# Performance work log

Hardware: AMD Instinct MI355X
Metric: run time of the kernel (lower is better)

The kernel has to match this reference:

```python
import jax, jax.numpy as jnp
import numpy as np
from jax.ops import segment_sum

N_NODES = 100000
N_EDGES = 1600000
N_GRAPHS = 128
HIDDEN = 128
N_CLASSES = 10


def setup_inputs() -> dict:
    key = jax.random.key(0)
    ks = jax.random.split(key, 8)
    src = jax.random.randint(ks[0], (N_EDGES,), 0, N_NODES, dtype=jnp.int32)
    dst = jax.random.randint(ks[1], (N_EDGES,), 0, N_NODES, dtype=jnp.int32)
    graph_ids = jnp.sort(jax.random.randint(ks[2], (N_NODES,), 0, N_GRAPHS, dtype=jnp.int32))
    W1 = jax.random.normal(ks[3], (1, HIDDEN), dtype=jnp.float32)
    b1 = jnp.zeros((HIDDEN,), jnp.float32)
    W2 = jax.random.normal(ks[4], (HIDDEN, HIDDEN), dtype=jnp.float32) * 0.05
    b2 = jnp.zeros((HIDDEN,), jnp.float32)
    Wc = jax.random.normal(ks[5], (HIDDEN, N_CLASSES), dtype=jnp.float32) * 0.05
    bc = jnp.zeros((N_CLASSES,), jnp.float32)
    return {"src": src, "dst": dst, "graph_ids": graph_ids,
            "W1": W1, "b1": b1, "W2": W2, "b2": b2, "Wc": Wc, "bc": bc}


def _graph_conv(h, src, dst, norm_src, norm_dst, W, b, n_nodes):
    # DGL GraphConv, norm='both': D_out^{-1/2} gather -> scatter-sum -> W -> D_in^{-1/2} -> +b
    hs = h * norm_src[:, None]
    agg = segment_sum(hs[src], dst, num_segments=n_nodes)  # [N, F_in]
    return agg @ W * norm_dst[:, None] + b


def reference(src, dst, graph_ids, W1, b1, W2, b2, Wc, bc):
    n_nodes = graph_ids.shape[0]
    ones_e = jnp.ones(src.shape[0], jnp.float32)
    indeg = segment_sum(ones_e, dst, num_segments=n_nodes)
    outdeg = segment_sum(ones_e, src, num_segments=n_nodes)
    norm_src = jnp.clip(outdeg, 1.0, None) ** -0.5
    norm_dst = jnp.clip(indeg, 1.0, None) ** -0.5

    h = indeg[:, None]  # node feature = in-degree, [N, 1]
    h = jax.nn.relu(_graph_conv(h, src, dst, norm_src, norm_dst, W1, b1, n_nodes))
    h = jax.nn.relu(_graph_conv(h, src, dst, norm_src, norm_dst, W2, b2, n_nodes))

    # dgl.mean_nodes: per-graph mean pooling
    sums = segment_sum(h, graph_ids, num_segments=N_GRAPHS)          # [G, H]
    cnts = segment_sum(jnp.ones(n_nodes, jnp.float32), graph_ids, num_segments=N_GRAPHS)
    hg = sums / jnp.clip(cnts, 1.0, None)[:, None]
    return hg @ Wc + bc  # [G, n_classes]
```

## Files before the change

kernel.cpp:

```cpp
#include <hip/hip_runtime.h>

#define N_NODES   100000
#define N_EDGES   1600000
#define N_GRAPHS  128
#define HIDDEN    128
#define N_CLASSES 10

#define BSH   8
#define BSZ   256
#define NBUCK 391
#define NBIN  512
#define CAP   8192
#define PCH   4096
#define PTH   512
#define PIT   (PCH / PTH)

typedef unsigned int   uint;
typedef unsigned short ushort;

__device__ __forceinline__ uint scan_excl_512(uint v, int t, uint* wtmp) {
    uint lane = (uint)(t & 63);
    uint incl = v;
    #pragma unroll
    for (int off = 1; off < 64; off <<= 1) {
        uint up = __shfl_up(incl, off, 64);
        if (lane >= (uint)off) incl += up;
    }
    if (lane == 63) wtmp[t >> 6] = incl;
    __syncthreads();
    uint wo = 0;
    int w = t >> 6;
    #pragma unroll
    for (int k = 0; k < 7; ++k) wo += (k < w) ? wtmp[k] : 0u;
    __syncthreads();
    return incl + wo - v;
}

__global__ __launch_bounds__(PTH)
void k_part(const int* __restrict__ src, const int* __restrict__ dst,
            uint* __restrict__ bcur1, uint* __restrict__ bcur2,
            uint* __restrict__ tmp1, ushort* __restrict__ tmp2, int nE) {
    __shared__ uint   hist[NBIN], lcur[NBIN], base[NBIN];
    __shared__ uint   wtmp[8];
    __shared__ uint   stag4[PCH];
    __shared__ ushort stagB[PCH];
    int t = threadIdx.x;
    int e0 = blockIdx.x * PCH;
    int e1 = min(e0 + PCH, nE);
    int cntE = e1 - e0;

    int sv[PIT], dv[PIT];
    hist[t] = 0;
    __syncthreads();
    #pragma unroll
    for (int m = 0; m < PIT; ++m) {
        int e = e0 + t + m * PTH;
        if (e < e1) {
            sv[m] = src[e]; dv[m] = dst[e];
            atomicAdd(&hist[dv[m] >> BSH], 1u);
        }
    }
    __syncthreads();
    uint v = hist[t];
    uint excl = scan_excl_512(v, t, wtmp);
    lcur[t] = excl;
    if (v > 0) { uint g = atomicAdd(&bcur1[t], v); base[t] = (uint)t * CAP + g - excl; }
    __syncthreads();
    #pragma unroll
    for (int m = 0; m < PIT; ++m) {
        int e = e0 + t + m * PTH;
        if (e < e1) {
            int d = dv[m], s = sv[m];
            int b = d >> BSH;
            uint p = atomicAdd(&lcur[b], 1u);
            stag4[p] = ((uint)(d & (BSZ - 1)) << 17) | (uint)s;
            stagB[p] = (ushort)b;
        }
    }
    __syncthreads();
    for (int i = t; i < cntE; i += PTH) {
        uint b = stagB[i];
        uint a = base[b] + (uint)i;
        if (a < (b + 1u) * CAP) tmp1[a] = stag4[i];
    }
    __syncthreads();

    hist[t] = 0;
    __syncthreads();
    #pragma unroll
    for (int m = 0; m < PIT; ++m) {
        int e = e0 + t + m * PTH;
        if (e < e1) atomicAdd(&hist[sv[m] >> BSH], 1u);
    }
    __syncthreads();
    v = hist[t];
    excl = scan_excl_512(v, t, wtmp);
    lcur[t] = excl;
    if (v > 0) { uint g = atomicAdd(&bcur2[t], v); base[t] = (uint)t * CAP + g - excl; }
    __syncthreads();
    #pragma unroll
    for (int m = 0; m < PIT; ++m) {
        int e = e0 + t + m * PTH;
        if (e < e1) {
            int s = sv[m];
            uint p = atomicAdd(&lcur[s >> BSH], 1u);
            stag4[p] = (uint)s;
        }
    }
    __syncthreads();
    for (int i = t; i < cntE; i += PTH) {
        uint s = stag4[i];
        uint b = s >> BSH;
        uint a = base[b] + (uint)i;
        if (a < (b + 1u) * CAP) tmp2[a] = (ushort)(s & (BSZ - 1));
    }
}

__global__ __launch_bounds__(1024)
void k_cnt(const uint* __restrict__ bcur1, const uint* __restrict__ tmp1,
           const uint* __restrict__ bcur2, const ushort* __restrict__ tmp2,
           float* __restrict__ ns, float* __restrict__ hs0, float* __restrict__ ndv) {
    __shared__ uint cin[BSZ], cout[BSZ];
    int b = blockIdx.x, t = threadIdx.x;
    if (t < BSZ) { cin[t] = 0; cout[t] = 0; }
    __syncthreads();
    uint f1 = min(bcur1[b], (uint)CAP);
    const uint* tp1 = tmp1 + (size_t)b * CAP;
    uint i = t;
    for (; i + 3072u < f1; i += 4096u) {
        uint a0 = tp1[i], a1 = tp1[i + 1024], a2 = tp1[i + 2048], a3 = tp1[i + 3072];
        atomicAdd(&cin[a0 >> 17], 1u); atomicAdd(&cin[a1 >> 17], 1u);
        atomicAdd(&cin[a2 >> 17], 1u); atomicAdd(&cin[a3 >> 17], 1u);
    }
    for (; i < f1; i += 1024u) atomicAdd(&cin[tp1[i] >> 17], 1u);
    uint f2 = min(bcur2[b], (uint)CAP);
    const ushort* tp2 = tmp2 + (size_t)b * CAP;
    i = t;
    for (; i + 3072u < f2; i += 4096u) {
        uint a0 = tp2[i], a1 = tp2[i + 1024], a2 = tp2[i + 2048], a3 = tp2[i + 3072];
        atomicAdd(&cout[a0], 1u); atomicAdd(&cout[a1], 1u);
        atomicAdd(&cout[a2], 1u); atomicAdd(&cout[a3], 1u);
    }
    for (; i < f2; i += 1024u) atomicAdd(&cout[tp2[i]], 1u);
    __syncthreads();
    if (t < BSZ) {
        int n = b * BSZ + t;
        if (n < N_NODES) {
            uint ci = cin[t];
            float nsv = rsqrtf(fmaxf((float)cout[t], 1.0f));
            ns[n]  = nsv;
            hs0[n] = (float)ci * nsv;
            ndv[n] = rsqrtf(fmaxf((float)ci, 1.0f));
        }
    }
}

__global__ __launch_bounds__(1024)
void k_info(const uint* __restrict__ bcur1, const uint* __restrict__ tmp1,
            const float* __restrict__ hs0, const float* __restrict__ ns,
            const float* __restrict__ ndv,
            const float* __restrict__ W1, const float* __restrict__ b1,
            const float* __restrict__ W2,
            float* __restrict__ U, float* __restrict__ V,
            float4* __restrict__ info) {
    __shared__ float agg[BSZ];
    __shared__ float stu[128];
    __shared__ float sts[128];
    int b = blockIdx.x, t = threadIdx.x;
    if (t < BSZ) agg[t] = 0.0f;
    if (t < 128) {
        float w = W1[t], bb = b1[t];
        stu[t] = (w != 0.0f) ? (-bb / w) : 1e30f;
    }
    __syncthreads();
    if (b < 129) {
        if (t < 128) sts[t] = stu[t];
        __syncthreads();
        for (int k = 2; k <= 128; k <<= 1) {
            for (int j = k >> 1; j > 0; j >>= 1) {
                if (t < 128) {
                    int ixj = t ^ j;
                    if (ixj > t) {
                        float a = sts[t], bb = sts[ixj];
                        bool up = ((t & k) == 0);
                        if (up ? (a > bb) : (a < bb)) { sts[t] = bb; sts[ixj] = a; }
                    }
                }
                __syncthreads();
            }
        }
        if (t < 128) {
            int sg = b;
            float a_rep;
            if (sg == 0)        a_rep = sts[0]   - 1.0f;
            else if (sg == 128) a_rep = sts[127] + 1.0f;
            else                a_rep = 0.5f * (sts[sg - 1] + sts[sg]);
            float u = 0.0f, vv = 0.0f;
            #pragma unroll 8
            for (int j = 0; j < 128; ++j) {
                float w  = W1[j], bb = b1[j];
                float w2 = W2[j * HIDDEN + t];
                bool on  = (a_rep * w + bb > 0.0f);
                u  += on ? w  * w2 : 0.0f;
                vv += on ? bb * w2 : 0.0f;
            }
            U[sg * HIDDEN + t] = u;
            V[sg * HIDDEN + t] = vv;
        }
    }
    uint f1 = min(bcur1[b], (uint)CAP);
    const uint* tp1 = tmp1 + (size_t)b * CAP;
    uint i = t;
    for (; i + 3072u < f1; i += 4096u) {
        uint e0 = tp1[i], e1 = tp1[i + 1024], e2 = tp1[i + 2048], e3 = tp1[i + 3072];
        float h0 = hs0[e0 & 0x1FFFFu], h1 = hs0[e1 & 0x1FFFFu];
        float h2 = hs0[e2 & 0x1FFFFu], h3 = hs0[e3 & 0x1FFFFu];
        atomicAdd(&agg[e0 >> 17], h0); atomicAdd(&agg[e1 >> 17], h1);
        atomicAdd(&agg[e2 >> 17], h2); atomicAdd(&agg[e3 >> 17], h3);
    }
    for (; i < f1; i += 1024u) {
        uint e = tp1[i];
        atomicAdd(&agg[e >> 17], hs0[e & 0x1FFFFu]);
    }
    __syncthreads();
    int n = b * BSZ + t;
    if (t < BSZ && n < N_NODES) {
        float nd = ndv[n];
        float av = agg[t] * nd;
        int sgp = 0;
        #pragma unroll 16
        for (int q = 0; q < 128; ++q) sgp += (stu[q] < av) ? 1 : 0;
        float nsv = ns[n];
        info[n] = make_float4(nsv * av, nsv, __int_as_float(sgp), nd);
    }
}

__global__ __launch_bounds__(1024)
void k_conv2(const uint* __restrict__ bcur1, const uint* __restrict__ tmp1,
             const float4* __restrict__ info, const float* __restrict__ ndv,
             const float* __restrict__ U, const float* __restrict__ V,
             const int* __restrict__ graph_ids, const float* __restrict__ b2,
             float* __restrict__ pool, float* __restrict__ cnt) {
    __shared__ float aggA[BSZ], aggB[BSZ];
    __shared__ uint  smn[BSZ], smx[BSZ];
    int b = blockIdx.x, t = threadIdx.x;
    if (t < BSZ) { aggA[t] = 0.0f; aggB[t] = 0.0f; smn[t] = 255u; smx[t] = 0u; }
    __syncthreads();
    uint f1 = min(bcur1[b], (uint)CAP);
    const uint* tp1 = tmp1 + (size_t)b * CAP;
    uint i = t;
    for (; i + 3072u < f1; i += 4096u) {
        uint e0 = tp1[i], e1 = tp1[i + 1024], e2 = tp1[i + 2048], e3 = tp1[i + 3072];
        float4 n0 = info[e0 & 0x1FFFFu];
        float4 n1 = info[e1 & 0x1FFFFu];
        float4 n2 = info[e2 & 0x1FFFFu];
        float4 n3 = info[e3 & 0x1FFFFu];
        uint d0 = e0 >> 17, d1 = e1 >> 17, d2 = e2 >> 17, d3 = e3 >> 17;
        atomicAdd(&aggA[d0], n0.x); atomicAdd(&aggB[d0], n0.y);
        atomicAdd(&aggA[d1], n1.x); atomicAdd(&aggB[d1], n1.y);
        atomicAdd(&aggA[d2], n2.x); atomicAdd(&aggB[d2], n2.y);
        atomicAdd(&aggA[d3], n3.x); atomicAdd(&aggB[d3], n3.y);
        uint s0 = (uint)__float_as_int(n0.z), s1 = (uint)__float_as_int(n1.z);
        uint s2 = (uint)__float_as_int(n2.z), s3 = (uint)__float_as_int(n3.z);
        atomicMin(&smn[d0], s0); atomicMax(&smx[d0], s0);
        atomicMin(&smn[d1], s1); atomicMax(&smx[d1], s1);
        atomicMin(&smn[d2], s2); atomicMax(&smx[d2], s2);
        atomicMin(&smn[d3], s3); atomicMax(&smx[d3], s3);
    }
    for (; i < f1; i += 1024u) {
        uint e = tp1[i];
        uint dl = e >> 17;
        float4 nf = info[e & 0x1FFFFu];
        atomicAdd(&aggA[dl], nf.x);
        atomicAdd(&aggB[dl], nf.y);
        uint sg = (uint)__float_as_int(nf.z);
        atomicMin(&smn[dl], sg);
        atomicMax(&smx[dl], sg);
    }
    __syncthreads();

    int d = t & 127, q = t >> 7;
    float bbd = b2[d];
    int base = b * BSZ;
    int nmax = min(BSZ, N_NODES - base);
    int gcur = -1; float racc = 0.0f, cl = 0.0f;
    for (int r = q; r < nmax; r += 8) {
        int n = base + r;
        uint mn = smn[r], mx = smx[r];
        float acc;
        if (mn >= mx) {
            uint sg = min(mn, 128u);
            acc = aggA[r] * U[sg * HIDDEN + d] + aggB[r] * V[sg * HIDDEN + d];
        } else {
            acc = 0.0f;
            for (uint k = 0; k < f1; ++k) {
                uint e = tp1[k];
                if ((e >> 17) == (uint)r) {
                    float4 nf = info[e & 0x1FFFFu];
                    uint sg = (uint)__float_as_int(nf.z);
                    acc += nf.x * U[sg * HIDDEN + d] + nf.y * V[sg * HIDDEN + d];
                }
            }
        }
        float nd = ndv[n];
        float row = fmaxf(nd * acc + bbd, 0.0f);
        int g = graph_ids[n];
        if (g != gcur) {
            if (gcur >= 0) {
                atomicAdd(&pool[gcur * HIDDEN + d], racc);
                if (d == 0) atomicAdd(&cnt[gcur], cl);
            }
            gcur = g; racc = 0.0f; cl = 0.0f;
        }
        racc += row; cl += 1.0f;
    }
    if (gcur >= 0) {
        atomicAdd(&pool[gcur * HIDDEN + d], racc);
        if (d == 0) atomicAdd(&cnt[gcur], cl);
    }
}

__global__ void k_final(const float* __restrict__ pool, const float* __restrict__ cnt,
                        const float* __restrict__ Wc, const float* __restrict__ bc,
                        float* __restrict__ out) {
    int t = blockIdx.x * blockDim.x + threadIdx.x;
    if (t >= N_GRAPHS * N_CLASSES) return;
    int g = t / N_CLASSES, c = t % N_CLASSES;
    float inv = 1.0f / fmaxf(cnt[g], 1.0f);
    float acc = bc[c];
    for (int j = 0; j < HIDDEN; ++j)
        acc += pool[g * HIDDEN + j] * inv * Wc[j * N_CLASSES + c];
    out[t] = acc;
}

extern "C" void kernel_launch(void* const* d_in, const int* in_sizes, int n_in,
                              void* d_out, int out_size, void* d_ws, size_t ws_size,
                              hipStream_t stream) {
    const int*   src       = (const int*)d_in[0];
    const int*   dst       = (const int*)d_in[1];
    const int*   graph_ids = (const int*)d_in[2];
    const float* W1        = (const float*)d_in[3];
    const float* b1        = (const float*)d_in[4];
    const float* W2        = (const float*)d_in[5];
    const float* b2        = (const float*)d_in[6];
    const float* Wc        = (const float*)d_in[7];
    const float* bc        = (const float*)d_in[8];
    float* out = (float*)d_out;

    char* ws = (char*)d_ws;
    size_t off = 0;
    auto alloc = [&](size_t elems) { void* p = ws + off; off += elems * 4; return p; };

    uint*  bcur1 = (uint*) alloc(NBIN);
    uint*  bcur2 = (uint*) alloc(NBIN);
    float* pool  = (float*)alloc(N_GRAPHS * HIDDEN);
    float* cnt   = (float*)alloc(N_GRAPHS);
    size_t zero_bytes = off;
    float4* info = (float4*)alloc((size_t)N_NODES * 4);
    uint*   tmp1 = (uint*)  alloc((size_t)NBUCK * CAP);
    ushort* tmp2 = (ushort*)alloc((size_t)NBUCK * CAP / 2);
    float*  nsA  = (float*) alloc(N_NODES);
    float*  hs0  = (float*) alloc(N_NODES);
    float*  ndv  = (float*) alloc(N_NODES);
    float*  U    = (float*) alloc(129 * HIDDEN);
    float*  V    = (float*) alloc(129 * HIDDEN);

    hipMemsetAsync(d_ws, 0, zero_bytes, stream);

    int pblocks = (N_EDGES + PCH - 1) / PCH;
    k_part <<<pblocks, PTH, 0, stream>>>(src, dst, bcur1, bcur2, tmp1, tmp2, N_EDGES);
    k_cnt  <<<NBUCK, 1024, 0, stream>>>(bcur1, tmp1, bcur2, tmp2, nsA, hs0, ndv);
    k_info <<<NBUCK, 1024, 0, stream>>>(bcur1, tmp1, hs0, nsA, ndv, W1, b1, W2, U, V, info);
    k_conv2<<<NBUCK, 1024, 0, stream>>>(bcur1, tmp1, info, ndv, U, V, graph_ids, b2, pool, cnt);
    k_final<<<(N_GRAPHS * N_CLASSES + 255) / 256, 256, 0, stream>>>(pool, cnt, Wc, bc, out);
}
```

Baseline: 175.0 us.

## Split per-bucket edge aggregation across four blocks and add separate node passes

Each 256-node bucket's edge list is now processed by four 256-thread blocks instead of one 1024-thread block. Partial results are merged into global per-node arrays with atomics, and separate node-wise kernels compute norms and per-node info. Pooling is moved to its own kernel over 128-node chunks, with shared-memory staging of per-graph partial sums. The goal is more blocks in flight across the CUs on a launch that had only 391 blocks. The cost is extra kernel launches, global atomics, and round trips of intermediate arrays through memory.

```diff
diff --git a/kernel.cpp b/kernel.cpp
--- a/kernel.cpp
+++ b/kernel.cpp
@@ -9,11 +9,13 @@
 #define BSH   8
 #define BSZ   256
 #define NBUCK 391
+#define NPAD  (NBUCK * BSZ)
 #define NBIN  512
 #define CAP   8192
 #define PCH   4096
 #define PTH   512
 #define PIT   (PCH / PTH)
+#define SPLIT 4
 
 typedef unsigned int   uint;
 typedef unsigned short ushort;
@@ -116,65 +118,55 @@
     }
 }
 
-__global__ __launch_bounds__(1024)
-void k_cnt(const uint* __restrict__ bcur1, const uint* __restrict__ tmp1,
-           const uint* __restrict__ bcur2, const ushort* __restrict__ tmp2,
-           float* __restrict__ ns, float* __restrict__ hs0, float* __restrict__ ndv) {
-    __shared__ uint cin[BSZ], cout[BSZ];
-    int b = blockIdx.x, t = threadIdx.x;
-    if (t < BSZ) { cin[t] = 0; cout[t] = 0; }
+__global__ __launch_bounds__(256)
+void k_cnt4(const uint* __restrict__ bcur1, const uint* __restrict__ tmp1,
+            const uint* __restrict__ bcur2, const ushort* __restrict__ tmp2,
+            uint* __restrict__ cin, uint* __restrict__ cout) {
+    __shared__ uint lin[BSZ], lout[BSZ];
+    int b = blockIdx.x >> 2, q = blockIdx.x & 3;
+    int t = threadIdx.x;
+    lin[t] = 0; lout[t] = 0;
     __syncthreads();
     uint f1 = min(bcur1[b], (uint)CAP);
+    uint lo = f1 * (uint)q / 4u, hi = f1 * (uint)(q + 1) / 4u;
     const uint* tp1 = tmp1 + (size_t)b * CAP;
-    uint i = t;
-    for (; i + 3072u < f1; i += 4096u) {
-        uint a0 = tp1[i], a1 = tp1[i + 1024], a2 = tp1[i + 2048], a3 = tp1[i + 3072];
-        atomicAdd(&cin[a0 >> 17], 1u); atomicAdd(&cin[a1 >> 17], 1u);
-        atomicAdd(&cin[a2 >> 17], 1u); atomicAdd(&cin[a3 >> 17], 1u);
-    }
-    for (; i < f1; i += 1024u) atomicAdd(&cin[tp1[i] >> 17], 1u);
+    uint i = lo + t;
+    for (; i + 768u < hi; i += 1024u) {
+        uint a0 = tp1[i], a1 = tp1[i + 256], a2 = tp1[i + 512], a3 = tp1[i + 768];
+        atomicAdd(&lin[a0 >> 17], 1u); atomicAdd(&lin[a1 >> 17], 1u);
+        atomicAdd(&lin[a2 >> 17], 1u); atomicAdd(&lin[a3 >> 17], 1u);
+    }
+    for (; i < hi; i += 256u) atomicAdd(&lin[tp1[i] >> 17], 1u);
+
     uint f2 = min(bcur2[b], (uint)CAP);
+    uint lo2 = f2 * (uint)q / 4u, hi2 = f2 * (uint)(q + 1) / 4u;
     const ushort* tp2 = tmp2 + (size_t)b * CAP;
-    i = t;
-    for (; i + 3072u < f2; i += 4096u) {
-        uint a0 = tp2[i], a1 = tp2[i + 1024], a2 = tp2[i + 2048], a3 = tp2[i + 3072];
-        atomicAdd(&cout[a0], 1u); atomicAdd(&cout[a1], 1u);
-        atomicAdd(&cout[a2], 1u); atomicAdd(&cout[a3], 1u);
-    }
-    for (; i < f2; i += 1024u) atomicAdd(&cout[tp2[i]], 1u);
-    __syncthreads();
-    if (t < BSZ) {
-        int n = b * BSZ + t;
-        if (n < N_NODES) {
-            uint ci = cin[t];
-            float nsv = rsqrtf(fmaxf((float)cout[t], 1.0f));
-            ns[n]  = nsv;
-            hs0[n] = (float)ci * nsv;
-            ndv[n] = rsqrtf(fmaxf((float)ci, 1.0f));
-        }
-    }
-}
-
-__global__ __launch_bounds__(1024)
-void k_info(const uint* __restrict__ bcur1, const uint* __restrict__ tmp1,
-            const float* __restrict__ hs0, const float* __restrict__ ns,
-            const float* __restrict__ ndv,
-            const float* __restrict__ W1, const float* __restrict__ b1,
-            const float* __restrict__ W2,
-            float* __restrict__ U, float* __restrict__ V,
-            float4* __restrict__ info) {
-    __shared__ float agg[BSZ];
-    __shared__ float stu[128];
+    i = lo2 + t;
+    for (; i + 768u < hi2; i += 1024u) {
+        uint a0 = tp2[i], a1 = tp2[i + 256], a2 = tp2[i + 512], a3 = tp2[i + 768];
+        atomicAdd(&lout[a0], 1u); atomicAdd(&lout[a1], 1u);
+        atomicAdd(&lout[a2], 1u); atomicAdd(&lout[a3], 1u);
+    }
+    for (; i < hi2; i += 256u) atomicAdd(&lout[tp2[i]], 1u);
+    __syncthreads();
+    int n = b * BSZ + t;
+    if (lin[t])  atomicAdd(&cin[n],  lin[t]);
+    if (lout[t]) atomicAdd(&cout[n], lout[t]);
+}
+
+__global__ __launch_bounds__(256)
+void k_node1(const uint* __restrict__ cin, const uint* __restrict__ cout,
+             const float* __restrict__ W1, const float* __restrict__ b1,
+             const float* __restrict__ W2,
+             float* __restrict__ ns, float* __restrict__ hs0, float* __restrict__ ndv,
+             float* __restrict__ aggC, float* __restrict__ U, float* __restrict__ V) {
     __shared__ float sts[128];
     int b = blockIdx.x, t = threadIdx.x;
-    if (t < BSZ) agg[t] = 0.0f;
-    if (t < 128) {
-        float w = W1[t], bb = b1[t];
-        stu[t] = (w != 0.0f) ? (-bb / w) : 1e30f;
-    }
-    __syncthreads();
     if (b < 129) {
-        if (t < 128) sts[t] = stu[t];
+        if (t < 128) {
+            float w = W1[t], bb = b1[t];
+            sts[t] = (w != 0.0f) ? (-bb / w) : 1e30f;
+        }
         __syncthreads();
         for (int k = 2; k <= 128; k <<= 1) {
             for (int j = k >> 1; j > 0; j >>= 1) {
@@ -208,115 +200,199 @@
             V[sg * HIDDEN + t] = vv;
         }
     }
+    int n = b * 256 + t;
+    uint ci = cin[n];
+    float nsv = rsqrtf(fmaxf((float)cout[n], 1.0f));
+    ns[n]   = nsv;
+    hs0[n]  = (float)ci * nsv;
+    ndv[n]  = rsqrtf(fmaxf((float)ci, 1.0f));
+    aggC[n] = 0.0f;
+}
+
+__global__ __launch_bounds__(256)
+void k_agg1(const uint* __restrict__ bcur1, const uint* __restrict__ tmp1,
+            const float* __restrict__ hs0, float* __restrict__ aggC) {
+    __shared__ float agg[BSZ];
+    int b = blockIdx.x >> 2, q = blockIdx.x & 3;
+    int t = threadIdx.x;
+    agg[t] = 0.0f;
+    __syncthreads();
     uint f1 = min(bcur1[b], (uint)CAP);
+    uint lo = f1 * (uint)q / 4u, hi = f1 * (uint)(q + 1) / 4u;
     const uint* tp1 = tmp1 + (size_t)b * CAP;
-    uint i = t;
-    for (; i + 3072u < f1; i += 4096u) {
-        uint e0 = tp1[i], e1 = tp1[i + 1024], e2 = tp1[i + 2048], e3 = tp1[i + 3072];
+    uint i = lo + t;
+    for (; i + 768u < hi; i += 1024u) {
+        uint e0 = tp1[i], e1 = tp1[i + 256], e2 = tp1[i + 512], e3 = tp1[i + 768];
         float h0 = hs0[e0 & 0x1FFFFu], h1 = hs0[e1 & 0x1FFFFu];
         float h2 = hs0[e2 & 0x1FFFFu], h3 = hs0[e3 & 0x1FFFFu];
         atomicAdd(&agg[e0 >> 17], h0); atomicAdd(&agg[e1 >> 17], h1);
         atomicAdd(&agg[e2 >> 17], h2); atomicAdd(&agg[e3 >> 17], h3);
     }
-    for (; i < f1; i += 1024u) {
+    for (; i < hi; i += 256u) {
         uint e = tp1[i];
         atomicAdd(&agg[e >> 17], hs0[e & 0x1FFFFu]);
     }
     __syncthreads();
-    int n = b * BSZ + t;
-    if (t < BSZ && n < N_NODES) {
-        float nd = ndv[n];
-        float av = agg[t] * nd;
-        int sgp = 0;
-        #pragma unroll 16
-        for (int q = 0; q < 128; ++q) sgp += (stu[q] < av) ? 1 : 0;
-        float nsv = ns[n];
-        info[n] = make_float4(nsv * av, nsv, __int_as_float(sgp), nd);
-    }
-}
-
-__global__ __launch_bounds__(1024)
-void k_conv2(const uint* __restrict__ bcur1, const uint* __restrict__ tmp1,
-             const float4* __restrict__ info, const float* __restrict__ ndv,
-             const float* __restrict__ U, const float* __restrict__ V,
-             const int* __restrict__ graph_ids, const float* __restrict__ b2,
-             float* __restrict__ pool, float* __restrict__ cnt) {
-    __shared__ float aggA[BSZ], aggB[BSZ];
-    __shared__ uint  smn[BSZ], smx[BSZ];
-    int b = blockIdx.x, t = threadIdx.x;
-    if (t < BSZ) { aggA[t] = 0.0f; aggB[t] = 0.0f; smn[t] = 255u; smx[t] = 0u; }
+    if (agg[t] != 0.0f) atomicAdd(&aggC[b * BSZ + t], agg[t]);
+}
+
+__global__ __launch_bounds__(256)
+void k_node2(const float* __restrict__ aggC, const float* __restrict__ ns,
+             const float* __restrict__ ndv,
+             const float* __restrict__ W1, const float* __restrict__ b1,
+             float4* __restrict__ info, float* __restrict__ aggA,
+             float* __restrict__ aggB, uint* __restrict__ aggMn,
+             uint* __restrict__ aggMx) {
+    __shared__ float stu[128];
+    int t = threadIdx.x;
+    if (t < 128) {
+        float w = W1[t], bb = b1[t];
+        stu[t] = (w != 0.0f) ? (-bb / w) : 1e30f;
+    }
+    __syncthreads();
+    int n = blockIdx.x * 256 + t;
+    float nd = ndv[n];
+    float av = aggC[n] * nd;
+    int sgp = 0;
+    #pragma unroll 16
+    for (int q = 0; q < 128; ++q) sgp += (stu[q] < av) ? 1 : 0;
+    float nsv = ns[n];
+    info[n] = make_float4(nsv * av, nsv, __int_as_float(sgp), nd);
+    aggA[n] = 0.0f; aggB[n] = 0.0f; aggMn[n] = 255u; aggMx[n] = 0u;
+}
+
+__global__ __launch_bounds__(256)
+void k_agg2(const uint* __restrict__ bcur1, const uint* __restrict__ tmp1,
+            const float4* __restrict__ info,
+            float* __restrict__ aggA, float* __restrict__ aggB,
+            uint* __restrict__ aggMn, uint* __restrict__ aggMx) {
+    __shared__ float lA[BSZ], lB[BSZ];
+    __shared__ uint  lmn[BSZ], lmx[BSZ];
+    int b = blockIdx.x >> 2, q = blockIdx.x & 3;
+    int t = threadIdx.x;
+    lA[t] = 0.0f; lB[t] = 0.0f; lmn[t] = 255u; lmx[t] = 0u;
     __syncthreads();
     uint f1 = min(bcur1[b], (uint)CAP);
+    uint lo = f1 * (uint)q / 4u, hi = f1 * (uint)(q + 1) / 4u;
     const uint* tp1 = tmp1 + (size_t)b * CAP;
-    uint i = t;
-    for (; i + 3072u < f1; i += 4096u) {
-        uint e0 = tp1[i], e1 = tp1[i + 1024], e2 = tp1[i + 2048], e3 = tp1[i + 3072];
+    uint i = lo + t;
+    for (; i + 768u < hi; i += 1024u) {
+        uint e0 = tp1[i], e1 = tp1[i + 256], e2 = tp1[i + 512], e3 = tp1[i + 768];
         float4 n0 = info[e0 & 0x1FFFFu];
         float4 n1 = info[e1 & 0x1FFFFu];
         float4 n2 = info[e2 & 0x1FFFFu];
         float4 n3 = info[e3 & 0x1FFFFu];
         uint d0 = e0 >> 17, d1 = e1 >> 17, d2 = e2 >> 17, d3 = e3 >> 17;
-        atomicAdd(&aggA[d0], n0.x); atomicAdd(&aggB[d0], n0.y);
-        atomicAdd(&aggA[d1], n1.x); atomicAdd(&aggB[d1], n1.y);
-        atomicAdd(&aggA[d2], n2.x); atomicAdd(&aggB[d2], n2.y);
-        atomicAdd(&aggA[d3], n3.x); atomicAdd(&aggB[d3], n3.y);
+        atomicAdd(&lA[d0], n0.x); atomicAdd(&lB[d0], n0.y);
+        atomicAdd(&lA[d1], n1.x); atomicAdd(&lB[d1], n1.y);
+        atomicAdd(&lA[d2], n2.x); atomicAdd(&lB[d2], n2.y);
+        atomicAdd(&lA[d3], n3.x); atomicAdd(&lB[d3], n3.y);
         uint s0 = (uint)__float_as_int(n0.z), s1 = (uint)__float_as_int(n1.z);
         uint s2 = (uint)__float_as_int(n2.z), s3 = (uint)__float_as_int(n3.z);
-        atomicMin(&smn[d0], s0); atomicMax(&smx[d0], s0);
-        atomicMin(&smn[d1], s1); atomicMax(&smx[d1], s1);
-        atomicMin(&smn[d2], s2); atomicMax(&smx[d2], s2);
-        atomicMin(&smn[d3], s3); atomicMax(&smx[d3], s3);
-    }
-    for (; i < f1; i += 1024u) {
+        atomicMin(&lmn[d0], s0); atomicMax(&lmx[d0], s0);
+        atomicMin(&lmn[d1], s1); atomicMax(&lmx[d1], s1);
+        atomicMin(&lmn[d2], s2); atomicMax(&lmx[d2], s2);
+        atomicMin(&lmn[d3], s3); atomicMax(&lmx[d3], s3);
+    }
+    for (; i < hi; i += 256u) {
         uint e = tp1[i];
         uint dl = e >> 17;
         float4 nf = info[e & 0x1FFFFu];
-        atomicAdd(&aggA[dl], nf.x);
-        atomicAdd(&aggB[dl], nf.y);
+        atomicAdd(&lA[dl], nf.x);
+        atomicAdd(&lB[dl], nf.y);
         uint sg = (uint)__float_as_int(nf.z);
-        atomicMin(&smn[dl], sg);
-        atomicMax(&smx[dl], sg);
-    }
-    __syncthreads();
-
-    int d = t & 127, q = t >> 7;
-    float bbd = b2[d];
-    int base = b * BSZ;
-    int nmax = min(BSZ, N_NODES - base);
+        atomicMin(&lmn[dl], sg);
+        atomicMax(&lmx[dl], sg);
+    }
+    __syncthreads();
+    if (lmn[t] <= lmx[t]) {
+        int n = b * BSZ + t;
+        atomicAdd(&aggA[n], lA[t]);
+        atomicAdd(&aggB[n], lB[t]);
+        atomicMin(&aggMn[n], lmn[t]);
+        atomicMax(&aggMx[n], lmx[t]);
+    }
+}
+
+__global__ __launch_bounds__(256)
+void k_pool(const uint* __restrict__ bcur1, const uint* __restrict__ tmp1,
+            const float4* __restrict__ info, const float* __restrict__ ndv,
+            const float* __restrict__ aggA, const float* __restrict__ aggB,
+            const uint* __restrict__ aggMn, const uint* __restrict__ aggMx,
+            const float* __restrict__ U, const float* __restrict__ V,
+            const int* __restrict__ graph_ids, const float* __restrict__ b2,
+            float* __restrict__ pool, float* __restrict__ cnt) {
+    __shared__ float psl[4][HIDDEN];
+    __shared__ float csl[4];
+    __shared__ uint  tfl[4];
+    __shared__ int   g0s;
+    int t = threadIdx.x;
+    int d = t & 127, j = t >> 7;
+    int nb = blockIdx.x * 128;
+    if (t < 4) { csl[t] = 0.0f; tfl[t] = 0u; }
+    for (int s = t; s < 4 * HIDDEN; s += 256) ((float*)psl)[s] = 0.0f;
+    if (t == 0) g0s = graph_ids[nb];
+    __syncthreads();
+    int g0 = g0s;
+    float b2d = b2[d];
     int gcur = -1; float racc = 0.0f, cl = 0.0f;
-    for (int r = q; r < nmax; r += 8) {
-        int n = base + r;
-        uint mn = smn[r], mx = smx[r];
+    for (int r = j; r < 128; r += 2) {
+        int n = nb + r;
+        if (n >= N_NODES) break;
+        uint mn = aggMn[n], mx = aggMx[n];
         float acc;
         if (mn >= mx) {
             uint sg = min(mn, 128u);
-            acc = aggA[r] * U[sg * HIDDEN + d] + aggB[r] * V[sg * HIDDEN + d];
+            acc = aggA[n] * U[sg * HIDDEN + d] + aggB[n] * V[sg * HIDDEN + d];
         } else {
             acc = 0.0f;
+            int bb = n >> BSH;
+            uint f1 = min(bcur1[bb], (uint)CAP);
+            const uint* tp1 = tmp1 + (size_t)bb * CAP;
+            uint dl = (uint)(n & (BSZ - 1));
             for (uint k = 0; k < f1; ++k) {
                 uint e = tp1[k];
-                if ((e >> 17) == (uint)r) {
+                if ((e >> 17) == dl) {
                     float4 nf = info[e & 0x1FFFFu];
                     uint sg = (uint)__float_as_int(nf.z);
                     acc += nf.x * U[sg * HIDDEN + d] + nf.y * V[sg * HIDDEN + d];
                 }
             }
         }
-        float nd = ndv[n];
-        float row = fmaxf(nd * acc + bbd, 0.0f);
+        float row = fmaxf(ndv[n] * acc + b2d, 0.0f);
         int g = graph_ids[n];
         if (g != gcur) {
             if (gcur >= 0) {
-                atomicAdd(&pool[gcur * HIDDEN + d], racc);
-                if (d == 0) atomicAdd(&cnt[gcur], cl);
+                int slot = gcur - g0;
+                if (slot >= 0 && slot < 4) {
+                    atomicAdd(&psl[slot][d], racc);
+                    if (d == 0) { atomicAdd(&csl[slot], cl); tfl[slot] = 1u; }
+                } else {
+                    atomicAdd(&pool[gcur * HIDDEN + d], racc);
+                    if (d == 0) atomicAdd(&cnt[gcur], cl);
+                }
             }
             gcur = g; racc = 0.0f; cl = 0.0f;
         }
         racc += row; cl += 1.0f;
     }
     if (gcur >= 0) {
-        atomicAdd(&pool[gcur * HIDDEN + d], racc);
-        if (d == 0) atomicAdd(&cnt[gcur], cl);
+        int slot = gcur - g0;
+        if (slot >= 0 && slot < 4) {
+            atomicAdd(&psl[slot][d], racc);
+            if (d == 0) { atomicAdd(&csl[slot], cl); tfl[slot] = 1u; }
+        } else {
+            atomicAdd(&pool[gcur * HIDDEN + d], racc);
+            if (d == 0) atomicAdd(&cnt[gcur], cl);
+        }
+    }
+    __syncthreads();
+    #pragma unroll
+    for (int s = 0; s < 4; ++s) {
+        if (tfl[s]) {
+            if (t < 128) atomicAdd(&pool[(g0 + s) * HIDDEN + t], psl[s][t]);
+            if (t == 128) atomicAdd(&cnt[g0 + s], csl[s]);
+        }
     }
 }
 
@@ -355,22 +431,37 @@
     uint*  bcur2 = (uint*) alloc(NBIN);
     float* pool  = (float*)alloc(N_GRAPHS * HIDDEN);
     float* cnt   = (float*)alloc(N_GRAPHS);
+    uint*  cin   = (uint*) alloc(NPAD);
+    uint*  cout  = (uint*) alloc(NPAD);
     size_t zero_bytes = off;
-    float4* info = (float4*)alloc((size_t)N_NODES * 4);
-    uint*   tmp1 = (uint*)  alloc((size_t)NBUCK * CAP);
-    ushort* tmp2 = (ushort*)alloc((size_t)NBUCK * CAP / 2);
-    float*  nsA  = (float*) alloc(N_NODES);
-    float*  hs0  = (float*) alloc(N_NODES);
-    float*  ndv  = (float*) alloc(N_NODES);
-    float*  U    = (float*) alloc(129 * HIDDEN);
-    float*  V    = (float*) alloc(129 * HIDDEN);
+    float4* info  = (float4*)alloc((size_t)NPAD * 4);
+    uint*   tmp1  = (uint*)  alloc((size_t)NBUCK * CAP);
+    ushort* tmp2  = (ushort*)alloc((size_t)NBUCK * CAP / 2);
+    float*  nsA   = (float*) alloc(NPAD);
+    float*  hs0   = (float*) alloc(NPAD);
+    float*  ndv   = (float*) alloc(NPAD);
+    float*  aggC  = (float*) alloc(NPAD);
+    float*  aggA  = (float*) alloc(NPAD);
+    float*  aggB  = (float*) alloc(NPAD);
+    uint*   aggMn = (uint*)  alloc(NPAD);
+    uint*   aggMx = (uint*)  alloc(NPAD);
+    float*  U     = (float*) alloc(129 * HIDDEN);
+    float*  V     = (float*) alloc(129 * HIDDEN);
 
     hipMemsetAsync(d_ws, 0, zero_bytes, stream);
 
     int pblocks = (N_EDGES + PCH - 1) / PCH;
+    int gblocks = NBUCK * SPLIT;
+    int nblocks = NPAD / 256;
+    int oblocks = NPAD / 128;
+
     k_part <<<pblocks, PTH, 0, stream>>>(src, dst, bcur1, bcur2, tmp1, tmp2, N_EDGES);
-    k_cnt  <<<NBUCK, 1024, 0, stream>>>(bcur1, tmp1, bcur2, tmp2, nsA, hs0, ndv);
-    k_info <<<NBUCK, 1024, 0, stream>>>(bcur1, tmp1, hs0, nsA, ndv, W1, b1, W2, U, V, info);
-    k_conv2<<<NBUCK, 1024, 0, stream>>>(bcur1, tmp1, info, ndv, U, V, graph_ids, b2, pool, cnt);
+    k_cnt4 <<<gblocks, 256, 0, stream>>>(bcur1, tmp1, bcur2, tmp2, cin, cout);
+    k_node1<<<nblocks, 256, 0, stream>>>(cin, cout, W1, b1, W2, nsA, hs0, ndv, aggC, U, V);
+    k_agg1 <<<gblocks, 256, 0, stream>>>(bcur1, tmp1, hs0, aggC);
+    k_node2<<<nblocks, 256, 0, stream>>>(aggC, nsA, ndv, W1, b1, info, aggA, aggB, aggMn, aggMx);
+    k_agg2 <<<gblocks, 256, 0, stream>>>(bcur1, tmp1, info, aggA, aggB, aggMn, aggMx);
+    k_pool <<<oblocks, 256, 0, stream>>>(bcur1, tmp1, info, ndv, aggA, aggB, aggMn, aggMx,
+                                         U, V, graph_ids, b2, pool, cnt);
     k_final<<<(N_GRAPHS * N_CLASSES + 255) / 256, 256, 0, stream>>>(pool, cnt, Wc, bc, out);
 }
```

Measured after the change: 188.8 us. 1.08x slower.

## Shrink node buckets to 64 nodes and pack out-degree indices into bytes

Applied to the files above, without the earlier changes.

Cuts the destination/source bucket size from 256 to 64 nodes, giving 1563 buckets. The count, info and conv2 kernels now launch with 256 threads instead of 1024, so there are about four times as many blocks to spread across the GPU's compute units. The partition kernel now scans 2048 bins, four per thread. Out-degree local indices become single bytes and are read four at a time as packed words. The trade-off is more global bucket-cursor atomics and more fragmented scatter writes in the partition step, plus a lower per-bucket capacity that leaves less headroom for skewed degree distributions.

```diff
diff --git a/kernel.cpp b/kernel.cpp
--- a/kernel.cpp
+++ b/kernel.cpp
@@ -6,17 +6,19 @@
 #define HIDDEN    128
 #define N_CLASSES 10
 
-#define BSH   8
-#define BSZ   256
-#define NBUCK 391
-#define NBIN  512
-#define CAP   8192
+#define BSH   6
+#define BSZ   64
+#define NBUCK 1563
+#define NPAD  (NBUCK * BSZ)
+#define NBIN  2048
+#define CAP   2048
 #define PCH   4096
 #define PTH   512
 #define PIT   (PCH / PTH)
 
 typedef unsigned int   uint;
 typedef unsigned short ushort;
+typedef unsigned char  uchar;
 
 __device__ __forceinline__ uint scan_excl_512(uint v, int t, uint* wtmp) {
     uint lane = (uint)(t & 63);
@@ -39,7 +41,7 @@
 __global__ __launch_bounds__(PTH)
 void k_part(const int* __restrict__ src, const int* __restrict__ dst,
             uint* __restrict__ bcur1, uint* __restrict__ bcur2,
-            uint* __restrict__ tmp1, ushort* __restrict__ tmp2, int nE) {
+            uint* __restrict__ tmp1, uchar* __restrict__ tmp2, int nE) {
     __shared__ uint   hist[NBIN], lcur[NBIN], base[NBIN];
     __shared__ uint   wtmp[8];
     __shared__ uint   stag4[PCH];
@@ -50,7 +52,7 @@
     int cntE = e1 - e0;
 
     int sv[PIT], dv[PIT];
-    hist[t] = 0;
+    hist[t] = 0; hist[t + 512] = 0; hist[t + 1024] = 0; hist[t + 1536] = 0;
     __syncthreads();
     #pragma unroll
     for (int m = 0; m < PIT; ++m) {
@@ -61,10 +63,17 @@
         }
     }
     __syncthreads();
-    uint v = hist[t];
-    uint excl = scan_excl_512(v, t, wtmp);
-    lcur[t] = excl;
-    if (v > 0) { uint g = atomicAdd(&bcur1[t], v); base[t] = (uint)t * CAP + g - excl; }
+    {
+        uint v0 = hist[4*t], v1 = hist[4*t+1], v2 = hist[4*t+2], v3 = hist[4*t+3];
+        uint ssum = v0 + v1 + v2 + v3;
+        uint ex = scan_excl_512(ssum, t, wtmp);
+        uint l0 = ex, l1 = ex + v0, l2 = l1 + v1, l3 = l2 + v2;
+        lcur[4*t] = l0; lcur[4*t+1] = l1; lcur[4*t+2] = l2; lcur[4*t+3] = l3;
+        if (v0) { uint g = atomicAdd(&bcur1[4*t+0], v0); base[4*t+0] = (uint)(4*t+0) * CAP + g - l0; }
+        if (v1) { uint g = atomicAdd(&bcur1[4*t+1], v1); base[4*t+1] = (uint)(4*t+1) * CAP + g - l1; }
+        if (v2) { uint g = atomicAdd(&bcur1[4*t+2], v2); base[4*t+2] = (uint)(4*t+2) * CAP + g - l2; }
+        if (v3) { uint g = atomicAdd(&bcur1[4*t+3], v3); base[4*t+3] = (uint)(4*t+3) * CAP + g - l3; }
+    }
     __syncthreads();
     #pragma unroll
     for (int m = 0; m < PIT; ++m) {
@@ -85,7 +94,7 @@
     }
     __syncthreads();
 
-    hist[t] = 0;
+    hist[t] = 0; hist[t + 512] = 0; hist[t + 1024] = 0; hist[t + 1536] = 0;
     __syncthreads();
     #pragma unroll
     for (int m = 0; m < PIT; ++m) {
@@ -93,10 +102,17 @@
         if (e < e1) atomicAdd(&hist[sv[m] >> BSH], 1u);
     }
     __syncthreads();
-    v = hist[t];
-    excl = scan_excl_512(v, t, wtmp);
-    lcur[t] = excl;
-    if (v > 0) { uint g = atomicAdd(&bcur2[t], v); base[t] = (uint)t * CAP + g - excl; }
+    {
+        uint v0 = hist[4*t], v1 = hist[4*t+1], v2 = hist[4*t+2], v3 = hist[4*t+3];
+        uint ssum = v0 + v1 + v2 + v3;
+        uint ex = scan_excl_512(ssum, t, wtmp);
+        uint l0 = ex, l1 = ex + v0, l2 = l1 + v1, l3 = l2 + v2;
+        lcur[4*t] = l0; lcur[4*t+1] = l1; lcur[4*t+2] = l2; lcur[4*t+3] = l3;
+        if (v0) { uint g = atomicAdd(&bcur2[4*t+0], v0); base[4*t+0] = (uint)(4*t+0) * CAP + g - l0; }
+        if (v1) { uint g = atomicAdd(&bcur2[4*t+1], v1); base[4*t+1] = (uint)(4*t+1) * CAP + g - l1; }
+        if (v2) { uint g = atomicAdd(&bcur2[4*t+2], v2); base[4*t+2] = (uint)(4*t+2) * CAP + g - l2; }
+        if (v3) { uint g = atomicAdd(&bcur2[4*t+3], v3); base[4*t+3] = (uint)(4*t+3) * CAP + g - l3; }
+    }
     __syncthreads();
     #pragma unroll
     for (int m = 0; m < PIT; ++m) {
@@ -112,13 +128,13 @@
         uint s = stag4[i];
         uint b = s >> BSH;
         uint a = base[b] + (uint)i;
-        if (a < (b + 1u) * CAP) tmp2[a] = (ushort)(s & (BSZ - 1));
-    }
-}
-
-__global__ __launch_bounds__(1024)
+        if (a < (b + 1u) * CAP) tmp2[a] = (uchar)(s & (BSZ - 1));
+    }
+}
+
+__global__ __launch_bounds__(256)
 void k_cnt(const uint* __restrict__ bcur1, const uint* __restrict__ tmp1,
-           const uint* __restrict__ bcur2, const ushort* __restrict__ tmp2,
+           const uint* __restrict__ bcur2, const uchar* __restrict__ tmp2,
            float* __restrict__ ns, float* __restrict__ hs0, float* __restrict__ ndv) {
     __shared__ uint cin[BSZ], cout[BSZ];
     int b = blockIdx.x, t = threadIdx.x;
@@ -127,21 +143,25 @@
     uint f1 = min(bcur1[b], (uint)CAP);
     const uint* tp1 = tmp1 + (size_t)b * CAP;
     uint i = t;
-    for (; i + 3072u < f1; i += 4096u) {
-        uint a0 = tp1[i], a1 = tp1[i + 1024], a2 = tp1[i + 2048], a3 = tp1[i + 3072];
+    for (; i + 768u < f1; i += 1024u) {
+        uint a0 = tp1[i], a1 = tp1[i + 256], a2 = tp1[i + 512], a3 = tp1[i + 768];
         atomicAdd(&cin[a0 >> 17], 1u); atomicAdd(&cin[a1 >> 17], 1u);
         atomicAdd(&cin[a2 >> 17], 1u); atomicAdd(&cin[a3 >> 17], 1u);
     }
-    for (; i < f1; i += 1024u) atomicAdd(&cin[tp1[i] >> 17], 1u);
+    for (; i < f1; i += 256u) atomicAdd(&cin[tp1[i] >> 17], 1u);
+
     uint f2 = min(bcur2[b], (uint)CAP);
-    const ushort* tp2 = tmp2 + (size_t)b * CAP;
-    i = t;
-    for (; i + 3072u < f2; i += 4096u) {
-        uint a0 = tp2[i], a1 = tp2[i + 1024], a2 = tp2[i + 2048], a3 = tp2[i + 3072];
-        atomicAdd(&cout[a0], 1u); atomicAdd(&cout[a1], 1u);
-        atomicAdd(&cout[a2], 1u); atomicAdd(&cout[a3], 1u);
-    }
-    for (; i < f2; i += 1024u) atomicAdd(&cout[tp2[i]], 1u);
+    const uchar* tp2 = tmp2 + (size_t)b * CAP;
+    const uint* tp2w = (const uint*)tp2;
+    uint nw = f2 >> 2;
+    for (i = t; i < nw; i += 256u) {
+        uint w4 = tp2w[i];
+        atomicAdd(&cout[w4 & 63u], 1u);
+        atomicAdd(&cout[(w4 >> 8) & 63u], 1u);
+        atomicAdd(&cout[(w4 >> 16) & 63u], 1u);
+        atomicAdd(&cout[(w4 >> 24) & 63u], 1u);
+    }
+    for (i = (nw << 2) + t; i < f2; i += 256u) atomicAdd(&cout[tp2[i]], 1u);
     __syncthreads();
     if (t < BSZ) {
         int n = b * BSZ + t;
@@ -155,7 +175,7 @@
     }
 }
 
-__global__ __launch_bounds__(1024)
+__global__ __launch_bounds__(256)
 void k_info(const uint* __restrict__ bcur1, const uint* __restrict__ tmp1,
             const float* __restrict__ hs0, const float* __restrict__ ns,
             const float* __restrict__ ndv,
@@ -211,86 +231,88 @@
     uint f1 = min(bcur1[b], (uint)CAP);
     const uint* tp1 = tmp1 + (size_t)b * CAP;
     uint i = t;
-    for (; i + 3072u < f1; i += 4096u) {
-        uint e0 = tp1[i], e1 = tp1[i + 1024], e2 = tp1[i + 2048], e3 = tp1[i + 3072];
+    for (; i + 768u < f1; i += 1024u) {
+        uint e0 = tp1[i], e1 = tp1[i + 256], e2 = tp1[i + 512], e3 = tp1[i + 768];
         float h0 = hs0[e0 & 0x1FFFFu], h1 = hs0[e1 & 0x1FFFFu];
         float h2 = hs0[e2 & 0x1FFFFu], h3 = hs0[e3 & 0x1FFFFu];
         atomicAdd(&agg[e0 >> 17], h0); atomicAdd(&agg[e1 >> 17], h1);
         atomicAdd(&agg[e2 >> 17], h2); atomicAdd(&agg[e3 >> 17], h3);
     }
-    for (; i < f1; i += 1024u) {
+    for (; i < f1; i += 256u) {
         uint e = tp1[i];
         atomicAdd(&agg[e >> 17], hs0[e & 0x1FFFFu]);
     }
     __syncthreads();
-    int n = b * BSZ + t;
-    if (t < BSZ && n < N_NODES) {
-        float nd = ndv[n];
-        float av = agg[t] * nd;
-        int sgp = 0;
-        #pragma unroll 16
-        for (int q = 0; q < 128; ++q) sgp += (stu[q] < av) ? 1 : 0;
-        float nsv = ns[n];
-        info[n] = make_float4(nsv * av, nsv, __int_as_float(sgp), nd);
-    }
-}
-
-__global__ __launch_bounds__(1024)
+    if (t < BSZ) {
+        int n = b * BSZ + t;
+        if (n < N_NODES) {
+            float nd = ndv[n];
+            float av = agg[t] * nd;
+            int sgp = 0;
+            #pragma unroll 16
+            for (int q = 0; q < 128; ++q) sgp += (stu[q] < av) ? 1 : 0;
+            float nsv = ns[n];
+            info[n] = make_float4(nsv * av, nsv, __int_as_float(sgp), nd);
+        }
+    }
+}
+
+__global__ __launch_bounds__(256)
 void k_conv2(const uint* __restrict__ bcur1, const uint* __restrict__ tmp1,
              const float4* __restrict__ info, const float* __restrict__ ndv,
              const float* __restrict__ U, const float* __restrict__ V,
              const int* __restrict__ graph_ids, const float* __restrict__ b2,
              float* __restrict__ pool, float* __restrict__ cnt) {
-    __shared__ float aggA[BSZ], aggB[BSZ];
-    __shared__ uint  smn[BSZ], smx[BSZ];
+    __shared__ float lA[BSZ], lB[BSZ];
+    __shared__ uint  lmn[BSZ], lmx[BSZ];
     int b = blockIdx.x, t = threadIdx.x;
-    if (t < BSZ) { aggA[t] = 0.0f; aggB[t] = 0.0f; smn[t] = 255u; smx[t] = 0u; }
+    if (t < BSZ) { lA[t] = 0.0f; lB[t] = 0.0f; lmn[t] = 255u; lmx[t] = 0u; }
     __syncthreads();
     uint f1 = min(bcur1[b], (uint)CAP);
     const uint* tp1 = tmp1 + (size_t)b * CAP;
     uint i = t;
-    for (; i + 3072u < f1; i += 4096u) {
-        uint e0 = tp1[i], e1 = tp1[i + 1024], e2 = tp1[i + 2048], e3 = tp1[i + 3072];
+    for (; i + 768u < f1; i += 1024u) {
+        uint e0 = tp1[i], e1 = tp1[i + 256], e2 = tp1[i + 512], e3 = tp1[i + 768];
         float4 n0 = info[e0 & 0x1FFFFu];
         float4 n1 = info[e1 & 0x1FFFFu];
         float4 n2 = info[e2 & 0x1FFFFu];
         float4 n3 = info[e3 & 0x1FFFFu];
         uint d0 = e0 >> 17, d1 = e1 >> 17, d2 = e2 >> 17, d3 = e3 >> 17;
-        atomicAdd(&aggA[d0], n0.x); atomicAdd(&aggB[d0], n0.y);
-        atomicAdd(&aggA[d1], n1.x); atomicAdd(&aggB[d1], n1.y);
-        atomicAdd(&aggA[d2], n2.x); atomicAdd(&aggB[d2], n2.y);
-        atomicAdd(&aggA[d3], n3.x); atomicAdd(&aggB[d3], n3.y);
+        atomicAdd(&lA[d0], n0.x); atomicAdd(&lB[d0], n0.y);
+        atomicAdd(&lA[d1], n1.x); atomicAdd(&lB[d1], n1.y);
+        atomicAdd(&lA[d2], n2.x); atomicAdd(&lB[d2], n2.y);
+        atomicAdd(&lA[d3], n3.x); atomicAdd(&lB[d3], n3.y);
         uint s0 = (uint)__float_as_int(n0.z), s1 = (uint)__float_as_int(n1.z);
         uint s2 = (uint)__float_as_int(n2.z), s3 = (uint)__float_as_int(n3.z);
-        atomicMin(&smn[d0], s0); atomicMax(&smx[d0], s0);
-        atomicMin(&smn[d1], s1); atomicMax(&smx[d1], s1);
-        atomicMin(&smn[d2], s2); atomicMax(&smx[d2], s2);
-        atomicMin(&smn[d3], s3); atomicMax(&smx[d3], s3);
-    }
-    for (; i < f1; i += 1024u) {
+        atomicMin(&lmn[d0], s0); atomicMax(&lmx[d0], s0);
+        atomicMin(&lmn[d1], s1); atomicMax(&lmx[d1], s1);
+        atomicMin(&lmn[d2], s2); atomicMax(&lmx[d2], s2);
+        atomicMin(&lmn[d3], s3); atomicMax(&lmx[d3], s3);
+    }
+    for (; i < f1; i += 256u) {
         uint e = tp1[i];
         uint dl = e >> 17;
         float4 nf = info[e & 0x1FFFFu];
-        atomicAdd(&aggA[dl], nf.x);
-        atomicAdd(&aggB[dl], nf.y);
+        atomicAdd(&lA[dl], nf.x);
+        atomicAdd(&lB[dl], nf.y);
         uint sg = (uint)__float_as_int(nf.z);
-        atomicMin(&smn[dl], sg);
-        atomicMax(&smx[dl], sg);
-    }
-    __syncthreads();
-
-    int d = t & 127, q = t >> 7;
+        atomicMin(&lmn[dl], sg);
+        atomicMax(&lmx[dl], sg);
+    }
+    __syncthreads();
+
+    int d = t & 127, j = t >> 7;
     float bbd = b2[d];
     int base = b * BSZ;
-    int nmax = min(BSZ, N_NODES - base);
     int gcur = -1; float racc = 0.0f, cl = 0.0f;
-    for (int r = q; r < nmax; r += 8) {
+    for (int r = j; r < BSZ; r += 2) {
         int n = base + r;
-        uint mn = smn[r], mx = smx[r];
+        if (n >= N_NODES) break;
+        uint mn = lmn[r], mx = lmx[r];
         float acc;
         if (mn >= mx) {
             uint sg = min(mn, 128u);
-            acc = aggA[r] * U[sg * HIDDEN + d] + aggB[r] * V[sg * HIDDEN + d];
+            acc = lA[r] * U[sg * HIDDEN + d] + lB[r] * V[sg * HIDDEN + d];
         } else {
             acc = 0.0f;
             for (uint k = 0; k < f1; ++k) {
@@ -302,8 +324,7 @@
                 }
             }
         }
-        float nd = ndv[n];
-        float row = fmaxf(nd * acc + bbd, 0.0f);
+        float row = fmaxf(ndv[n] * acc + bbd, 0.0f);
         int g = graph_ids[n];
         if (g != gcur) {
             if (gcur >= 0) {
@@ -356,12 +377,12 @@
     float* pool  = (float*)alloc(N_GRAPHS * HIDDEN);
     float* cnt   = (float*)alloc(N_GRAPHS);
     size_t zero_bytes = off;
-    float4* info = (float4*)alloc((size_t)N_NODES * 4);
+    float4* info = (float4*)alloc((size_t)NPAD * 4);
     uint*   tmp1 = (uint*)  alloc((size_t)NBUCK * CAP);
-    ushort* tmp2 = (ushort*)alloc((size_t)NBUCK * CAP / 2);
-    float*  nsA  = (float*) alloc(N_NODES);
-    float*  hs0  = (float*) alloc(N_NODES);
-    float*  ndv  = (float*) alloc(N_NODES);
+    uchar*  tmp2 = (uchar*) alloc((size_t)NBUCK * CAP / 4);
+    float*  nsA  = (float*) alloc(NPAD);
+    float*  hs0  = (float*) alloc(NPAD);
+    float*  ndv  = (float*) alloc(NPAD);
     float*  U    = (float*) alloc(129 * HIDDEN);
     float*  V    = (float*) alloc(129 * HIDDEN);
 
@@ -369,8 +390,8 @@
 
     int pblocks = (N_EDGES + PCH - 1) / PCH;
     k_part <<<pblocks, PTH, 0, stream>>>(src, dst, bcur1, bcur2, tmp1, tmp2, N_EDGES);
-    k_cnt  <<<NBUCK, 1024, 0, stream>>>(bcur1, tmp1, bcur2, tmp2, nsA, hs0, ndv);
-    k_info <<<NBUCK, 1024, 0, stream>>>(bcur1, tmp1, hs0, nsA, ndv, W1, b1, W2, U, V, info);
-    k_conv2<<<NBUCK, 1024, 0, stream>>>(bcur1, tmp1, info, ndv, U, V, graph_ids, b2, pool, cnt);
+    k_cnt  <<<NBUCK, 256, 0, stream>>>(bcur1, tmp1, bcur2, tmp2, nsA, hs0, ndv);
+    k_info <<<NBUCK, 256, 0, stream>>>(bcur1, tmp1, hs0, nsA, ndv, W1, b1, W2, U, V, info);
+    k_conv2<<<NBUCK, 256, 0, stream>>>(bcur1, tmp1, info, ndv, U, V, graph_ids, b2, pool, cnt);
     k_final<<<(N_GRAPHS * N_CLASSES + 255) / 256, 256, 0, stream>>>(pool, cnt, Wc, bc, out);
 }
```

After: 216.2 us. 23.5% more time.
